# Kernel tuning notes

Measured on AMD Instinct MI355X. Metric: run time of the kernel, lower is better.

## Reference

```python
import jax, jax.numpy as jnp
import numpy as np

E = 1024
H = 16
DH = E // H
EPS = 1e-09


def setup_inputs() -> dict:
    key = jax.random.key(0)
    ks = jax.random.split(key, 12)
    B, S = 2, 2048
    scale = 1.0 / np.sqrt(E)
    inp = {
        "query": jax.random.normal(ks[0], (B, S, E), dtype=jnp.float32),
        "key": jax.random.normal(ks[1], (B, S, E), dtype=jnp.float32),
        "value": jax.random.normal(ks[2], (B, S, E), dtype=jnp.float32),
        "mask": jax.random.randint(ks[3], (B, 1, S, S), 0, 2, dtype=jnp.int32),
        "Wq": jax.random.normal(ks[4], (E, E), dtype=jnp.float32) * scale,
        "bq": jnp.zeros((E,), dtype=jnp.float32),
        "Wk": jax.random.normal(ks[5], (E, E), dtype=jnp.float32) * scale,
        "bk": jnp.zeros((E,), dtype=jnp.float32),
        "Wv": jax.random.normal(ks[6], (E, E), dtype=jnp.float32) * scale,
        "bv": jnp.zeros((E,), dtype=jnp.float32),
        "Wo": jax.random.normal(ks[7], (E, E), dtype=jnp.float32) * scale,
        "bo": jnp.zeros((E,), dtype=jnp.float32),
    }
    return inp


def _split_heads(x):
    # [B,S,E] -> [B,H,S,DH]
    B, S, _ = x.shape
    return x.reshape(B, S, H, DH).transpose(0, 2, 1, 3)


def reference(query, key, value, mask, Wq, bq, Wk, bk, Wv, bv, Wo, bo):
    q = _split_heads(query @ Wq.T + bq)
    k = _split_heads(key @ Wk.T + bk)
    v = _split_heads(value @ Wv.T + bv)
    # scores: [B,H,Sq,Sk]; NOTE: original module applies NO softmax.
    scores = jnp.einsum("bhqd,bhkd->bhqk", q, k) / np.sqrt(DH)
    # masked_fill_(mask == 0, epsilon): replace masked positions with 1e-9
    scores = jnp.where(mask == 0, jnp.float32(EPS), scores)
    # dropout p=0.0 (eval) -> identity
    out = jnp.einsum("bhqk,bhkd->bhqd", scores, v)
    B, _, S, _ = out.shape
    out = out.transpose(0, 2, 1, 3).reshape(B, S, E)
    return out @ Wo.T + bo
```

## Files before the change

kernel.cpp:

```cpp
#include <hip/hip_runtime.h>
#include <hip/hip_bf16.h>
#include <stdint.h>
#include <stddef.h>

#define SB 2
#define SS 2048
#define SE 1024
#define SH 16
#define SD 64

typedef __attribute__((ext_vector_type(8))) short bf16x8;
typedef __attribute__((ext_vector_type(4))) float f32x4;

__device__ __forceinline__ short f2bf(float f) {
    union { float f; uint32_t u; } v; v.f = f;
    uint32_t u = v.u;
    uint32_t r = (u + 0x7fffu + ((u >> 16) & 1u)) >> 16;
    return (short)(uint16_t)r;
}

__device__ __forceinline__ float bf2f(short s) {
    union { uint32_t u; float f; } v;
    v.u = (uint32_t)(uint16_t)s << 16;
    return v.f;
}

__device__ __forceinline__ uint32_t pkmask(float a, float b, uint32_t bits) {
    union { float f; uint32_t u; } ua, ub;
    ua.f = a; ub.f = b;
    uint32_t ra = (bits & 1u) ? (ua.u + 0x7fffu + ((ua.u >> 16) & 1u)) : 0u;
    uint32_t rb = (bits & 2u) ? (ub.u + 0x7fffu + ((ub.u >> 16) & 1u)) : 0u;
    return (rb & 0xffff0000u) | (ra >> 16);
}

__device__ __forceinline__ void gld16(const short* g, short* l) {
    __builtin_amdgcn_global_load_lds(
        (const __attribute__((address_space(1))) unsigned int*)g,
        (__attribute__((address_space(3))) unsigned int*)l, 16, 0, 0);
}

struct CvtArgs {
    const float* src[7];
    short* dst[7];
    int nblk[7];
};

__global__ __launch_bounds__(256) void cvt_bf16(CvtArgs a) {
    const int j = blockIdx.y;
    if (blockIdx.x >= a.nblk[j]) return;
    const size_t i = ((size_t)blockIdx.x * 256 + threadIdx.x) * 8;
    const float* s = a.src[j] + i;
    f32x4 f0 = *(const f32x4*)s;
    f32x4 f1 = *(const f32x4*)(s + 4);
    bf16x8 o;
    o[0] = f2bf(f0[0]); o[1] = f2bf(f0[1]); o[2] = f2bf(f0[2]); o[3] = f2bf(f0[3]);
    o[4] = f2bf(f1[0]); o[5] = f2bf(f1[1]); o[6] = f2bf(f1[2]); o[7] = f2bf(f1[3]);
    *(bf16x8*)(a.dst[j] + i) = o;
}

__global__ __launch_bounds__(256) void pack_mask(const int* __restrict__ m,
                                                 unsigned long long* __restrict__ mp) {
    const int lane = threadIdx.x & 63;
    int wv = (blockIdx.x * 256 + threadIdx.x) >> 6;
    const int NW = SB * SS * (SS / 64);
    const int stride = (gridDim.x * 256) >> 6;
    for (int wd = wv; wd < NW; wd += stride) {
        int v = m[(size_t)wd * 64 + lane];
        unsigned long long bb = __ballot(v != 0);
        if (lane == 0) {
            int b = wd >> 16;
            int q = (wd >> 5) & 2047;
            int kw = wd & 31;
            mp[((size_t)b << 16) + kw * 2048 + q] = bb;
        }
    }
}

__global__ __launch_bounds__(256) void add_po(const short* __restrict__ p0,
                                              const short* __restrict__ p1,
                                              short* __restrict__ o) {
    const size_t i = ((size_t)blockIdx.x * 256 + threadIdx.x) * 8;
    bf16x8 a = *(const bf16x8*)(p0 + i);
    bf16x8 b = *(const bf16x8*)(p1 + i);
    bf16x8 r;
#pragma unroll
    for (int j = 0; j < 8; ++j) r[j] = f2bf(bf2f(a[j]) + bf2f(b[j]));
    *(bf16x8*)(o + i) = r;
}

struct GemmJob {
    const short* A; const short* W; const float* bias; void* C;
    int mode;
    float scale;
};

template <bool OUTF32>
__global__ __launch_bounds__(256, 3) void gemm128(GemmJob j0, GemmJob j1, GemmJob j2) {
    GemmJob j = (blockIdx.z == 0) ? j0 : (blockIdx.z == 1) ? j1 : j2;
    __shared__ short As[128 * 64];
    __shared__ short Bs[128 * 64];

    const int m0 = blockIdx.y * 128;
    const int n0 = blockIdx.x * 128;
    const int tid = threadIdx.x;
    const int lane = tid & 63;
    const int w = tid >> 6;
    const int wm = (w >> 1) * 64;
    const int wn = (w & 1) * 64;
    const int quad = lane >> 4;
    const int l16 = lane & 15;

    f32x4 acc[4][4] = {};

    for (int k0 = 0; k0 < 1024; k0 += 64) {
#pragma unroll
        for (int i = 0; i < 4; ++i) {
            int ch = lane + 64 * (w * 4 + i);
            int row = ch >> 3;
            int col = (ch & 7) * 8;
            gld16(j.A + (size_t)(m0 + row) * 1024 + k0 + col, &As[(w * 4 + i) * 512]);
            gld16(j.W + (size_t)(n0 + row) * 1024 + k0 + col, &Bs[(w * 4 + i) * 512]);
        }
        __syncthreads();
#pragma unroll
        for (int ks = 0; ks < 2; ++ks) {
            bf16x8 af[4], bfr[4];
#pragma unroll
            for (int mi = 0; mi < 4; ++mi)
                af[mi] = *(const bf16x8*)&As[(wm + mi * 16 + l16) * 64 + ks * 32 + quad * 8];
#pragma unroll
            for (int ni = 0; ni < 4; ++ni)
                bfr[ni] = *(const bf16x8*)&Bs[(wn + ni * 16 + l16) * 64 + ks * 32 + quad * 8];
#pragma unroll
            for (int mi = 0; mi < 4; ++mi)
#pragma unroll
                for (int ni = 0; ni < 4; ++ni)
                    acc[mi][ni] = __builtin_amdgcn_mfma_f32_16x16x32_bf16(
                        af[mi], bfr[ni], acc[mi][ni], 0, 0, 0);
        }
        __syncthreads();
    }

#pragma unroll
    for (int mi = 0; mi < 4; ++mi) {
#pragma unroll
        for (int ni = 0; ni < 4; ++ni) {
            int n = n0 + wn + ni * 16 + l16;
            float bv = j.bias[n];
#pragma unroll
            for (int r = 0; r < 4; ++r) {
                int m = m0 + wm + mi * 16 + quad * 4 + r;
                float v = (acc[mi][ni][r] + bv) * j.scale;
                if (OUTF32) {
                    ((float*)j.C)[(size_t)m * 1024 + n] = v;
                } else {
                    short o = f2bf(v);
                    short* C = (short*)j.C;
                    if (j.mode == 0) {
                        C[(size_t)m * 1024 + n] = o;
                    } else {
                        int b = m >> 11, s = m & 2047;
                        int hh = n >> 6, d = n & 63;
                        if (j.mode == 1)
                            C[(((size_t)(b * SH + hh) * SS) + s) * SD + d] = o;
                        else
                            C[(((size_t)(b * SH + hh) * SD) + d) * SS + s] = o;
                    }
                }
            }
        }
    }
}

__global__ __launch_bounds__(256, 4) void attn2(
    const short* __restrict__ Q,
    const short* __restrict__ Kk,
    const short* __restrict__ Vt,
    const unsigned long long* __restrict__ MpT,
    short* __restrict__ P0,
    short* __restrict__ P1) {
    __shared__ __align__(16) short Ks[2][64 * 72];
    __shared__ __align__(16) short Vs[2][64 * 72];

    const int qt = blockIdx.x;
    const int bh = blockIdx.y;
    const int b = bh >> 4;
    const int h = bh & 15;
    const int kbeg = blockIdx.z << 10;
    short* po = blockIdx.z ? P1 : P0;

    const short* qbase = Q + (size_t)bh * SS * SD;
    const short* kbase = Kk + (size_t)bh * SS * SD;
    const short* vbase = Vt + (size_t)bh * SD * SS;
    const unsigned long long* mTb = MpT + ((size_t)b << 16);

    const int tid = threadIdx.x;
    const int lane = tid & 63;
    const int w = tid >> 6;
    const int quad = lane >> 4;
    const int l16 = lane & 15;
    const int qw = qt * 128 + w * 32;

    bf16x8 qf[2][2];
#pragma unroll
    for (int u = 0; u < 2; ++u) {
        qf[u][0] = *(const bf16x8*)(qbase + (size_t)(qw + u * 16 + l16) * SD + quad * 8);
        qf[u][1] = *(const bf16x8*)(qbase + (size_t)(qw + u * 16 + l16) * SD + 32 + quad * 8);
    }

    f32x4 oacc[2][4] = {};

    bf16x8 kpf[2], vpf[2];
    int prow[2], pcol[2];
#pragma unroll
    for (int r = 0; r < 2; ++r) {
        int ch = tid + r * 256;
        prow[r] = ch >> 3;
        pcol[r] = (ch & 7) * 8;
    }
    auto loadKV = [&](int k0) {
#pragma unroll
        for (int r = 0; r < 2; ++r) {
            kpf[r] = *(const bf16x8*)(kbase + (size_t)(k0 + prow[r]) * SD + pcol[r]);
            vpf[r] = *(const bf16x8*)(vbase + (size_t)prow[r] * SS + k0 + pcol[r]);
        }
    };
    auto storeKV = [&](int buf) {
#pragma unroll
        for (int r = 0; r < 2; ++r) {
            *(bf16x8*)&Ks[buf][prow[r] * 72 + pcol[r]] = kpf[r];
            *(bf16x8*)&Vs[buf][prow[r] * 72 + pcol[r]] = vpf[r];
        }
    };

    loadKV(kbeg);
    int cur = 0;

    for (int k0 = kbeg; k0 < kbeg + 1024; k0 += 64) {
        storeKV(cur);
        if (k0 + 64 < kbeg + 1024) loadKV(k0 + 64);
        unsigned long long wq0 = mTb[(k0 >> 6) * 2048 + qw + l16];
        unsigned long long wq1 = mTb[(k0 >> 6) * 2048 + qw + 16 + l16];
        __syncthreads();

        const short* KsB = &Ks[cur][0];
        const short* VsB = &Vs[cur][0];
#pragma unroll
        for (int p = 0; p < 2; ++p) {
            const int s0 = p * 2, s1 = p * 2 + 1;
            bf16x8 a00 = *(const bf16x8*)&KsB[(s0 * 16 + l16) * 72 + quad * 8];
            bf16x8 a01 = *(const bf16x8*)&KsB[(s0 * 16 + l16) * 72 + 32 + quad * 8];
            bf16x8 a10 = *(const bf16x8*)&KsB[(s1 * 16 + l16) * 72 + quad * 8];
            bf16x8 a11 = *(const bf16x8*)&KsB[(s1 * 16 + l16) * 72 + 32 + quad * 8];

            union SCU { uint32_t d[4]; bf16x8 v; } scf[2];
#pragma unroll
            for (int u = 0; u < 2; ++u) {
                f32x4 sA = {}, sB = {};
                sA = __builtin_amdgcn_mfma_f32_16x16x32_bf16(a00, qf[u][0], sA, 0, 0, 0);
                sA = __builtin_amdgcn_mfma_f32_16x16x32_bf16(a01, qf[u][1], sA, 0, 0, 0);
                sB = __builtin_amdgcn_mfma_f32_16x16x32_bf16(a10, qf[u][0], sB, 0, 0, 0);
                sB = __builtin_amdgcn_mfma_f32_16x16x32_bf16(a11, qf[u][1], sB, 0, 0, 0);

                unsigned long long w64 = u ? wq1 : wq0;
                uint32_t sh0 = (uint32_t)(w64 >> (s0 * 16 + quad * 4));
                uint32_t sh1 = (uint32_t)(w64 >> (s1 * 16 + quad * 4));
                scf[u].d[0] = pkmask(sA[0], sA[1], sh0);
                scf[u].d[1] = pkmask(sA[2], sA[3], sh0 >> 2);
                scf[u].d[2] = pkmask(sB[0], sB[1], sh1);
                scf[u].d[3] = pkmask(sB[2], sB[3], sh1 >> 2);
            }

#pragma unroll
            for (int di = 0; di < 4; ++di) {
                union { uint32_t d[4]; bf16x8 v; } vb;
                const uint32_t* vlo =
                    (const uint32_t*)&VsB[(di * 16 + l16) * 72 + s0 * 16 + quad * 4];
                const uint32_t* vhi =
                    (const uint32_t*)&VsB[(di * 16 + l16) * 72 + s1 * 16 + quad * 4];
                vb.d[0] = vlo[0]; vb.d[1] = vlo[1];
                vb.d[2] = vhi[0]; vb.d[3] = vhi[1];
                oacc[0][di] = __builtin_amdgcn_mfma_f32_16x16x32_bf16(
                    scf[0].v, vb.v, oacc[0][di], 0, 0, 0);
                oacc[1][di] = __builtin_amdgcn_mfma_f32_16x16x32_bf16(
                    scf[1].v, vb.v, oacc[1][di], 0, 0, 0);
            }
        }
        cur ^= 1;
    }

#pragma unroll
    for (int u = 0; u < 2; ++u) {
#pragma unroll
        for (int di = 0; di < 4; ++di) {
            int d = di * 16 + l16;
#pragma unroll
            for (int r = 0; r < 4; ++r) {
                int qg2 = qw + u * 16 + quad * 4 + r;
                po[((size_t)b * SS + qg2) * SE + h * SD + d] = f2bf(oacc[u][di][r]);
            }
        }
    }
}

extern "C" void kernel_launch(void* const* d_in, const int* in_sizes, int n_in,
                              void* d_out, int out_size, void* d_ws,
                              size_t ws_size, hipStream_t stream) {
    const float* query = (const float*)d_in[0];
    const float* key   = (const float*)d_in[1];
    const float* value = (const float*)d_in[2];
    const int*   mask  = (const int*)d_in[3];
    float* out = (float*)d_out;

    const size_t NEL = (size_t)SB * SS * SE;
    unsigned long long* Mp = (unsigned long long*)d_out;
    short* mb   = (short*)d_in[3];
    short* qbf  = mb;
    short* kbf  = mb + NEL;
    short* vbf  = mb + 2 * NEL;
    short* Wqb  = mb + 3 * NEL;
    short* Wkb  = Wqb + SE * SE;
    short* Wvb  = Wkb + SE * SE;
    short* Wob  = Wvb + SE * SE;
    short* Qb   = (short*)d_in[0];
    short* P0   = Qb + NEL;
    short* Kb   = (short*)d_in[1];
    short* P1   = Kb + NEL;
    short* Vtb  = (short*)d_in[2];
    short* Om   = Vtb + NEL;

    dim3 tblk(256);

    pack_mask<<<dim3(1024), tblk, 0, stream>>>(mask, Mp);

    CvtArgs ca;
    ca.src[0] = query; ca.dst[0] = qbf; ca.nblk[0] = 2048;
    ca.src[1] = key;   ca.dst[1] = kbf; ca.nblk[1] = 2048;
    ca.src[2] = value; ca.dst[2] = vbf; ca.nblk[2] = 2048;
    ca.src[3] = (const float*)d_in[4];  ca.dst[3] = Wqb; ca.nblk[3] = 512;
    ca.src[4] = (const float*)d_in[6];  ca.dst[4] = Wkb; ca.nblk[4] = 512;
    ca.src[5] = (const float*)d_in[8];  ca.dst[5] = Wvb; ca.nblk[5] = 512;
    ca.src[6] = (const float*)d_in[10]; ca.dst[6] = Wob; ca.nblk[6] = 512;
    cvt_bf16<<<dim3(2048, 7), tblk, 0, stream>>>(ca);

    GemmJob jq{qbf, Wqb, (const float*)d_in[5], Qb,  1, 0.125f};
    GemmJob jv{vbf, Wvb, (const float*)d_in[9], Vtb, 2, 1.0f};
    GemmJob jk{kbf, Wkb, (const float*)d_in[7], Kb,  1, 1.0f};
    gemm128<false><<<dim3(8, 32, 3), tblk, 0, stream>>>(jq, jv, jk);

    attn2<<<dim3(SS / 128, SB * SH, 2), tblk, 0, stream>>>(Qb, Kb, Vtb, Mp, P0, P1);

    add_po<<<dim3(2048), tblk, 0, stream>>>(P0, P1, Om);

    gemm128<true><<<dim3(8, 32, 1), tblk, 0, stream>>>(
        GemmJob{Om, Wob, (const float*)d_in[11], out, 0, 1.0f},
        GemmJob{Om, Wob, (const float*)d_in[11], out, 0, 1.0f},
        GemmJob{Om, Wob, (const float*)d_in[11], out, 0, 1.0f});
}
```

Before: 275.7 us.

## Permute V^T layout for single 16-byte LDS loads, simplify mask and rounding

The V-transpose projection epilogue now writes each 64-element sequence block in a permuted order, so the attention kernel can fetch its V operand with one 128-bit LDS read instead of four 32-bit reads. Mask bits are pre-shifted once per tile, which removes per-iteration 64-bit shifts. The bf16 packing drops round-to-nearest-even and uses a plain round-half-up. s_setprio is raised around the MFMA section. The rounding change slightly alters numerics, and correctness depends on the permutation matching the MFMA k-index mapping.

```diff
diff --git a/kernel.cpp b/kernel.cpp
--- a/kernel.cpp
+++ b/kernel.cpp
@@ -28,8 +28,8 @@
 __device__ __forceinline__ uint32_t pkmask(float a, float b, uint32_t bits) {
     union { float f; uint32_t u; } ua, ub;
     ua.f = a; ub.f = b;
-    uint32_t ra = (bits & 1u) ? (ua.u + 0x7fffu + ((ua.u >> 16) & 1u)) : 0u;
-    uint32_t rb = (bits & 2u) ? (ub.u + 0x7fffu + ((ub.u >> 16) & 1u)) : 0u;
+    uint32_t ra = (bits & 1u) ? (ua.u + 0x8000u) : 0u;
+    uint32_t rb = (bits & 2u) ? (ub.u + 0x8000u) : 0u;
     return (rb & 0xffff0000u) | (ra >> 16);
 }
 
@@ -161,10 +161,15 @@
                     } else {
                         int b = m >> 11, s = m & 2047;
                         int hh = n >> 6, d = n & 63;
-                        if (j.mode == 1)
+                        if (j.mode == 1) {
                             C[(((size_t)(b * SH + hh) * SS) + s) * SD + d] = o;
-                        else
-                            C[(((size_t)(b * SH + hh) * SD) + d) * SS + s] = o;
+                        } else {
+                            int sl = s & 63;
+                            int sp = (sl & 0x20) | ((sl & 0x0C) << 1) |
+                                     ((sl & 0x10) >> 2) | (sl & 3);
+                            C[(((size_t)(b * SH + hh) * SD) + d) * SS +
+                              (s & ~63) + sp] = o;
+                        }
                     }
                 }
             }
@@ -245,6 +250,16 @@
 
         const short* KsB = &Ks[cur][0];
         const short* VsB = &Vs[cur][0];
+
+        uint32_t mlo[2], mhi[2];
+        {
+            unsigned long long W0 = wq0 >> (quad * 4);
+            unsigned long long W1 = wq1 >> (quad * 4);
+            mlo[0] = (uint32_t)W0; mhi[0] = (uint32_t)(W0 >> 32);
+            mlo[1] = (uint32_t)W1; mhi[1] = (uint32_t)(W1 >> 32);
+        }
+
+        __builtin_amdgcn_s_setprio(1);
 #pragma unroll
         for (int p = 0; p < 2; ++p) {
             const int s0 = p * 2, s1 = p * 2 + 1;
@@ -262,30 +277,23 @@
                 sB = __builtin_amdgcn_mfma_f32_16x16x32_bf16(a10, qf[u][0], sB, 0, 0, 0);
                 sB = __builtin_amdgcn_mfma_f32_16x16x32_bf16(a11, qf[u][1], sB, 0, 0, 0);
 
-                unsigned long long w64 = u ? wq1 : wq0;
-                uint32_t sh0 = (uint32_t)(w64 >> (s0 * 16 + quad * 4));
-                uint32_t sh1 = (uint32_t)(w64 >> (s1 * 16 + quad * 4));
-                scf[u].d[0] = pkmask(sA[0], sA[1], sh0);
-                scf[u].d[1] = pkmask(sA[2], sA[3], sh0 >> 2);
-                scf[u].d[2] = pkmask(sB[0], sB[1], sh1);
-                scf[u].d[3] = pkmask(sB[2], sB[3], sh1 >> 2);
+                uint32_t m0 = p ? mhi[u] : mlo[u];
+                scf[u].d[0] = pkmask(sA[0], sA[1], m0);
+                scf[u].d[1] = pkmask(sA[2], sA[3], m0 >> 2);
+                scf[u].d[2] = pkmask(sB[0], sB[1], m0 >> 16);
+                scf[u].d[3] = pkmask(sB[2], sB[3], m0 >> 18);
             }
 
 #pragma unroll
             for (int di = 0; di < 4; ++di) {
-                union { uint32_t d[4]; bf16x8 v; } vb;
-                const uint32_t* vlo =
-                    (const uint32_t*)&VsB[(di * 16 + l16) * 72 + s0 * 16 + quad * 4];
-                const uint32_t* vhi =
-                    (const uint32_t*)&VsB[(di * 16 + l16) * 72 + s1 * 16 + quad * 4];
-                vb.d[0] = vlo[0]; vb.d[1] = vlo[1];
-                vb.d[2] = vhi[0]; vb.d[3] = vhi[1];
+                bf16x8 vb = *(const bf16x8*)&VsB[(di * 16 + l16) * 72 + p * 32 + quad * 8];
                 oacc[0][di] = __builtin_amdgcn_mfma_f32_16x16x32_bf16(
-                    scf[0].v, vb.v, oacc[0][di], 0, 0, 0);
+                    scf[0].v, vb, oacc[0][di], 0, 0, 0);
                 oacc[1][di] = __builtin_amdgcn_mfma_f32_16x16x32_bf16(
-                    scf[1].v, vb.v, oacc[1][di], 0, 0, 0);
+                    scf[1].v, vb, oacc[1][di], 0, 0, 0);
             }
         }
+        __builtin_amdgcn_s_setprio(0);
         cur ^= 1;
     }
 
```

Result: no change. 271.5 us (-1.5%).
